# Optimization experiments

Measured on AMD Instinct MI355X. Metric: run time of the kernel, lower is better.

## Reference

```python
import jax, jax.numpy as jnp
import numpy as np

N_NODES = 50000
N_EDGES = 1000000
NODE_F = 64
EDGE_F = 64
OUT_F = 128
K = 2  # matches init k=2


def setup_inputs() -> dict:
    key = jax.random.key(0)
    k1, k2, k3, k4, k5, k6 = jax.random.split(key, 6)
    node_feat = jax.random.normal(k1, (N_NODES, NODE_F), dtype=jnp.float32)
    edge_feat = jax.random.normal(k2, (N_EDGES, EDGE_F), dtype=jnp.float32)
    # nn.Linear(edge_feats*2 + node_feats, out_feats): weight [out, in], bias [out]
    W = jax.random.normal(k3, (OUT_F, 2 * EDGE_F + NODE_F), dtype=jnp.float32) * 0.05
    b = jax.random.normal(k4, (OUT_F,), dtype=jnp.float32) * 0.05
    src = jax.random.randint(k5, (N_EDGES,), 0, N_NODES, dtype=jnp.int64)
    dst = jax.random.randint(k6, (N_EDGES,), 0, N_NODES, dtype=jnp.int64)
    return {"node_feat": node_feat, "edge_feat": edge_feat, "W": W, "b": b,
            "src": src, "dst": dst}


def reference(node_feat, edge_feat, W, b, src, dst):
    N = node_feat.shape[0]
    # norm = in_degrees().clamp(min=1) ** -0.5, shape [N, 1]
    deg = jax.ops.segment_sum(jnp.ones_like(dst, dtype=node_feat.dtype), dst,
                              num_segments=N)
    norm = jnp.maximum(deg, 1.0) ** -0.5
    norm = norm[:, None]
    # DGL semantics: update_all(copy_e, sum) overwrites ndata['h'] with the
    # scatter-sum of edge data over destination nodes; apply_edges then copies
    # the (un-normalized) node 'h' back to edges via edge.src.
    e = edge_feat  # [E, EDGE_F]
    fstack = [node_feat]
    for _ in range(K):
        h = jax.ops.segment_sum(e, dst, num_segments=N)  # [N, EDGE_F]
        fstack.append(h * norm)
        e = h[src]  # apply_edges: e = src node h (un-normalized)
    rst = jnp.concatenate(fstack, axis=-1) @ W.T + b  # [N, OUT_F]
    est = rst[src]  # final apply_edges copies lin output to edges
    return rst, est
```

## Files before the change

### kernel.cpp

```cpp
#include <hip/hip_runtime.h>
#include <hip/hip_bf16.h>

#define NF 64
#define N_OUT 128
#define CAT 192

typedef __attribute__((ext_vector_type(4))) float f32x4;
typedef __attribute__((ext_vector_type(8))) short bf16x8;

__device__ inline short f2bf(float x) {
  unsigned u = __float_as_uint(x);
  unsigned r = (u + 0x7fff + ((u >> 16) & 1)) >> 16;
  return (short)r;
}

__device__ inline f32x4 sx4(f32x4 v, int m) {
  f32x4 r;
  r.x = __shfl_xor(v.x, m, 64);
  r.y = __shfl_xor(v.y, m, 64);
  r.z = __shfl_xor(v.z, m, 64);
  r.w = __shfl_xor(v.w, m, 64);
  return r;
}

__global__ __launch_bounds__(256) void deg_kernel(const int* __restrict__ dst,
                                                  int* __restrict__ deg, int n_edges) {
  int i = blockIdx.x * blockDim.x + threadIdx.x;
  int stride = gridDim.x * blockDim.x;
  for (; i < n_edges; i += stride) {
    int d = __builtin_nontemporal_load(&dst[i]);
    atomicAdd(&deg[d], 1);
  }
}

__global__ __launch_bounds__(256) void scanA_kernel(const int* __restrict__ deg,
                                                    int* __restrict__ offs,
                                                    float* __restrict__ norm,
                                                    int* __restrict__ bsum, int n) {
  int tid = threadIdx.x;
  int i = blockIdx.x * 256 + tid;
  int lane = tid & 63, wid = tid >> 6;
  int v = (i < n) ? deg[i] : 0;
  int s = v;
  #pragma unroll
  for (int o = 1; o < 64; o <<= 1) {
    int t = __shfl_up(s, o, 64);
    if (lane >= o) s += t;
  }
  __shared__ int ws[4], wb[4];
  if (lane == 63) ws[wid] = s;
  __syncthreads();
  if (tid == 0) {
    int run = 0;
    #pragma unroll
    for (int w = 0; w < 4; ++w) { wb[w] = run; run += ws[w]; }
    bsum[blockIdx.x] = run;
  }
  __syncthreads();
  if (i < n) {
    offs[i] = wb[wid] + s - v;
    norm[i] = rsqrtf(fmaxf((float)v, 1.0f));
  }
}

__global__ __launch_bounds__(256) void scanB_kernel(int* __restrict__ bsum, int nb) {
  int tid = threadIdx.x, lane = tid & 63, wid = tid >> 6;
  int v = (tid < nb) ? bsum[tid] : 0;
  int s = v;
  #pragma unroll
  for (int o = 1; o < 64; o <<= 1) {
    int t = __shfl_up(s, o, 64);
    if (lane >= o) s += t;
  }
  __shared__ int ws[4], wb[4];
  if (lane == 63) ws[wid] = s;
  __syncthreads();
  if (tid == 0) {
    int run = 0;
    #pragma unroll
    for (int w = 0; w < 4; ++w) { wb[w] = run; run += ws[w]; }
  }
  __syncthreads();
  if (tid < nb) bsum[tid] = wb[wid] + s - v;
}

__global__ __launch_bounds__(256) void scanC_kernel(int* __restrict__ offs,
                                                    const int* __restrict__ bsum, int n) {
  int i = blockIdx.x * 256 + threadIdx.x;
  if (i < n) offs[i] += bsum[blockIdx.x];
}

__global__ __launch_bounds__(256) void fill_kernel(const int* __restrict__ src,
                                                   const int* __restrict__ dst,
                                                   int* __restrict__ offs,
                                                   int2* __restrict__ csr, int n_edges) {
  int i = blockIdx.x * blockDim.x + threadIdx.x;
  int stride = gridDim.x * blockDim.x;
  for (; i < n_edges; i += stride) {
    int d = __builtin_nontemporal_load(&dst[i]);
    int s = __builtin_nontemporal_load(&src[i]);
    int p = atomicAdd(&offs[d], 1);
    csr[p] = make_int2(i, s);
  }
}

__global__ __launch_bounds__(256) void h1_kernel(const float* __restrict__ edge_feat,
                                                 const int2* __restrict__ csr,
                                                 const int* __restrict__ offs,
                                                 float* __restrict__ h1, int n_nodes) {
  int n = blockIdx.x * 4 + (threadIdx.x >> 6);
  if (n >= n_nodes) return;
  int l = threadIdx.x & 63;
  int l15 = l & 15, l4 = l >> 4;
  int kb = n ? offs[n - 1] : 0;
  int ke = offs[n];
  f32x4 acc0 = {0.f, 0.f, 0.f, 0.f}, acc1 = {0.f, 0.f, 0.f, 0.f};
  int k = kb;
  for (; k + 8 <= ke; k += 8) {
    int e0 = csr[k + l4].x;
    int e1 = csr[k + 4 + l4].x;
    f32x4 v0 = __builtin_nontemporal_load((const f32x4*)&edge_feat[(size_t)e0 * NF + l15 * 4]);
    f32x4 v1 = __builtin_nontemporal_load((const f32x4*)&edge_feat[(size_t)e1 * NF + l15 * 4]);
    acc0 += v0;
    acc1 += v1;
  }
  if (k + 4 <= ke) {
    int e = csr[k + l4].x;
    acc0 += __builtin_nontemporal_load((const f32x4*)&edge_feat[(size_t)e * NF + l15 * 4]);
    k += 4;
  }
  int rem = ke - k;
  if (l4 < rem) {
    int e = csr[k + l4].x;
    acc1 += __builtin_nontemporal_load((const f32x4*)&edge_feat[(size_t)e * NF + l15 * 4]);
  }
  f32x4 t = acc0 + acc1;
  t += sx4(t, 16);
  t += sx4(t, 32);
  if (l4 == 0) *(f32x4*)&h1[(size_t)n * NF + l15 * 4] = t;
}

__global__ __launch_bounds__(256) void h2_kernel(const float* __restrict__ h1,
                                                 const int2* __restrict__ csr,
                                                 const int* __restrict__ offs,
                                                 float* __restrict__ h2, int n_nodes) {
  int n = blockIdx.x * 4 + (threadIdx.x >> 6);
  if (n >= n_nodes) return;
  int l = threadIdx.x & 63;
  int l15 = l & 15, l4 = l >> 4;
  int kb = n ? offs[n - 1] : 0;
  int ke = offs[n];
  f32x4 acc0 = {0.f, 0.f, 0.f, 0.f}, acc1 = {0.f, 0.f, 0.f, 0.f};
  int k = kb;
  for (; k + 8 <= ke; k += 8) {
    int s0 = csr[k + l4].y;
    int s1 = csr[k + 4 + l4].y;
    acc0 += *(const f32x4*)&h1[(size_t)s0 * NF + l15 * 4];
    acc1 += *(const f32x4*)&h1[(size_t)s1 * NF + l15 * 4];
  }
  if (k + 4 <= ke) {
    int s = csr[k + l4].y;
    acc0 += *(const f32x4*)&h1[(size_t)s * NF + l15 * 4];
    k += 4;
  }
  int rem = ke - k;
  if (l4 < rem) {
    int s = csr[k + l4].y;
    acc1 += *(const f32x4*)&h1[(size_t)s * NF + l15 * 4];
  }
  f32x4 t = acc0 + acc1;
  t += sx4(t, 16);
  t += sx4(t, 32);
  if (l4 == 0) *(f32x4*)&h2[(size_t)n * NF + l15 * 4] = t;
}

__global__ __launch_bounds__(256) void gemm_kernel(const float* __restrict__ node_feat,
                                                   const float* __restrict__ h1,
                                                   const float* __restrict__ h2,
                                                   const float* __restrict__ norm,
                                                   const float* __restrict__ W,
                                                   const float* __restrict__ bias,
                                                   float* __restrict__ rst,
                                                   short* __restrict__ rstb, int n_nodes) {
  __shared__ short F[32 * 200];
  __shared__ float R[32][132];
  int tid = threadIdx.x;
  int l = tid & 63, w = tid >> 6;
  int l15 = l & 15, l4 = l >> 4;

  bf16x8 Bf[6][2];
  #pragma unroll
  for (int c = 0; c < 2; ++c) {
    int col = w * 32 + c * 16 + l15;
    const float* wp = &W[(size_t)col * CAT];
    #pragma unroll
    for (int ks = 0; ks < 6; ++ks) {
      int k0 = ks * 32 + l4 * 8;
      bf16x8 b;
      #pragma unroll
      for (int j = 0; j < 8; ++j) b[j] = f2bf(wp[k0 + j]);
      Bf[ks][c] = b;
    }
  }
  float bias0 = bias[w * 32 + l15];
  float bias1 = bias[w * 32 + 16 + l15];

  int tiles = (n_nodes + 31) / 32;
  for (int tile = blockIdx.x; tile < tiles; tile += gridDim.x) {
    int nbase = tile * 32;
    __syncthreads();
    for (int idx = tid; idx < 768; idx += 256) {
      int m = idx / 24, q = idx - m * 24;
      int n = nbase + m;
      bf16x8 pk;
      if (n < n_nodes) {
        const float* sp;
        float scale = 1.f;
        if (q < 8)       sp = &node_feat[(size_t)n * NF + q * 8];
        else if (q < 16) { sp = &h1[(size_t)n * NF + (q - 8) * 8]; scale = norm[n]; }
        else             { sp = &h2[(size_t)n * NF + (q - 16) * 8]; scale = norm[n]; }
        f32x4 v0 = *(const f32x4*)sp;
        f32x4 v1 = *(const f32x4*)(sp + 4);
        pk[0] = f2bf(v0.x * scale); pk[1] = f2bf(v0.y * scale);
        pk[2] = f2bf(v0.z * scale); pk[3] = f2bf(v0.w * scale);
        pk[4] = f2bf(v1.x * scale); pk[5] = f2bf(v1.y * scale);
        pk[6] = f2bf(v1.z * scale); pk[7] = f2bf(v1.w * scale);
      } else {
        pk = bf16x8{0,0,0,0,0,0,0,0};
      }
      *(bf16x8*)&F[m * 200 + q * 8] = pk;
    }
    __syncthreads();
    f32x4 acc00 = {0.f,0.f,0.f,0.f}, acc01 = {0.f,0.f,0.f,0.f};
    f32x4 acc10 = {0.f,0.f,0.f,0.f}, acc11 = {0.f,0.f,0.f,0.f};
    #pragma unroll
    for (int ks = 0; ks < 6; ++ks) {
      bf16x8 a0 = *(const bf16x8*)&F[l15 * 200 + ks * 32 + l4 * 8];
      bf16x8 a1 = *(const bf16x8*)&F[(16 + l15) * 200 + ks * 32 + l4 * 8];
      acc00 = __builtin_amdgcn_mfma_f32_16x16x32_bf16(a0, Bf[ks][0], acc00, 0, 0, 0);
      acc01 = __builtin_amdgcn_mfma_f32_16x16x32_bf16(a0, Bf[ks][1], acc01, 0, 0, 0);
      acc10 = __builtin_amdgcn_mfma_f32_16x16x32_bf16(a1, Bf[ks][0], acc10, 0, 0, 0);
      acc11 = __builtin_amdgcn_mfma_f32_16x16x32_bf16(a1, Bf[ks][1], acc11, 0, 0, 0);
    }
    #pragma unroll
    for (int rt = 0; rt < 2; ++rt) {
      f32x4 ac0 = rt ? acc10 : acc00;
      f32x4 ac1 = rt ? acc11 : acc01;
      #pragma unroll
      for (int r = 0; r < 4; ++r) {
        int row = rt * 16 + l4 * 4 + r;
        R[row][w * 32 + l15] = ac0[r] + bias0;
        R[row][w * 32 + 16 + l15] = ac1[r] + bias1;
      }
    }
    __syncthreads();
    for (int idx = tid; idx < 32 * 32; idx += 256) {
      int m = idx >> 5, c = idx & 31;
      int n = nbase + m;
      if (n < n_nodes) {
        f32x4 v = *(const f32x4*)&R[m][c * 4];
        __builtin_nontemporal_store(v, (f32x4*)&rst[(size_t)n * N_OUT + c * 4]);
      }
    }
    if (rstb) {
      for (int idx = tid; idx < 32 * 16; idx += 256) {
        int m = idx >> 4, q = idx & 15;
        int n = nbase + m;
        if (n < n_nodes) {
          const float* rp = &R[m][q * 8];
          bf16x8 pk;
          #pragma unroll
          for (int j = 0; j < 8; ++j) pk[j] = f2bf(rp[j]);
          *(bf16x8*)&rstb[(size_t)n * N_OUT + q * 8] = pk;
        }
      }
    }
  }
}

__global__ __launch_bounds__(256) void est_bf16_kernel(const short* __restrict__ rstb,
                                                       const int* __restrict__ src,
                                                       float* __restrict__ est, int n_edges) {
  f32x4* e4 = (f32x4*)est;
  int total = n_edges * 32;
  int i = blockIdx.x * blockDim.x + threadIdx.x;
  int stride = gridDim.x * blockDim.x;
  for (; i < total; i += stride) {
    int e = i >> 5, c = i & 31;
    ushort4 b = *(const ushort4*)&rstb[(size_t)src[e] * N_OUT + c * 4];
    f32x4 v;
    v.x = __uint_as_float((unsigned)b.x << 16);
    v.y = __uint_as_float((unsigned)b.y << 16);
    v.z = __uint_as_float((unsigned)b.z << 16);
    v.w = __uint_as_float((unsigned)b.w << 16);
    __builtin_nontemporal_store(v, &e4[i]);
  }
}

__global__ __launch_bounds__(256) void est_f32_kernel(const float* __restrict__ rst,
                                                      const int* __restrict__ src,
                                                      float* __restrict__ est, int n_edges) {
  const f32x4* r4 = (const f32x4*)rst;
  f32x4* e4 = (f32x4*)est;
  int total = n_edges * 32;
  int i = blockIdx.x * blockDim.x + threadIdx.x;
  int stride = gridDim.x * blockDim.x;
  for (; i < total; i += stride) {
    int e = i >> 5, c = i & 31;
    f32x4 v = r4[(size_t)src[e] * 32 + c];
    __builtin_nontemporal_store(v, &e4[i]);
  }
}

extern "C" void kernel_launch(void* const* d_in, const int* in_sizes, int n_in,
                              void* d_out, int out_size, void* d_ws, size_t ws_size,
                              hipStream_t stream) {
  const float* node_feat = (const float*)d_in[0];
  const float* edge_feat = (const float*)d_in[1];
  const float* W = (const float*)d_in[2];
  const float* bias = (const float*)d_in[3];
  const int* src = (const int*)d_in[4];
  const int* dst = (const int*)d_in[5];
  int n_nodes = in_sizes[0] / NF;
  int n_edges = in_sizes[4];

  size_t off = 0;
  auto take = [&](size_t bytes) -> void* {
    void* p = (char*)d_ws + off;
    off += (bytes + 255) & ~(size_t)255;
    return p;
  };
  int* deg = (int*)take((size_t)n_nodes * 4);
  int* offs = (int*)take(((size_t)n_nodes + 1) * 4);
  float* norm = (float*)take((size_t)n_nodes * 4);
  int* bsum = (int*)take(256 * 4);
  int2* csr = (int2*)take((size_t)n_edges * 8);
  float* h1 = (float*)take((size_t)n_nodes * NF * 4);
  float* h2 = (float*)take((size_t)n_nodes * NF * 4);
  size_t rstb_bytes = (size_t)n_nodes * N_OUT * 2;
  short* rstb = nullptr;
  if (off + rstb_bytes <= ws_size) rstb = (short*)take(rstb_bytes);

  float* rst = (float*)d_out;
  float* est = rst + (size_t)n_nodes * N_OUT;

  hipMemsetAsync(deg, 0, (size_t)n_nodes * 4, stream);

  deg_kernel<<<2048, 256, 0, stream>>>(dst, deg, n_edges);
  int nbs = (n_nodes + 255) / 256;
  scanA_kernel<<<nbs, 256, 0, stream>>>(deg, offs, norm, bsum, n_nodes);
  scanB_kernel<<<1, 256, 0, stream>>>(bsum, nbs);
  scanC_kernel<<<nbs, 256, 0, stream>>>(offs, bsum, n_nodes);
  fill_kernel<<<2048, 256, 0, stream>>>(src, dst, offs, csr, n_edges);
  int nb = (n_nodes + 3) / 4;
  h1_kernel<<<nb, 256, 0, stream>>>(edge_feat, csr, offs, h1, n_nodes);
  h2_kernel<<<nb, 256, 0, stream>>>(h1, csr, offs, h2, n_nodes);
  gemm_kernel<<<320, 256, 0, stream>>>(node_feat, h1, h2, norm, W, bias,
                                       rst, rstb, n_nodes);
  if (rstb)
    est_bf16_kernel<<<4096, 256, 0, stream>>>(rstb, src, est, n_edges);
  else
    est_f32_kernel<<<4096, 256, 0, stream>>>(rst, src, est, n_edges);
}
```

Baseline: 389.2 us.

## Fuse scan phases, unroll gathers wider, enlarge GEMM tiles, retune grids

Merges the block-sum scan and offset fixup into one kernel, where each block redundantly rescans the block sums. This removes one launch. Packs CSR entries as 64-bit values written with nontemporal stores. Unrolls the h1/h2 gather loops to 16 edges with four accumulators so more loads are in flight. Doubles the GEMM tile to 64 rows with 512-thread blocks and raises the est grid size, at the cost of more LDS and register pressure per block.

```diff
diff --git a/kernel.cpp b/kernel.cpp
--- a/kernel.cpp
+++ b/kernel.cpp
@@ -63,7 +63,8 @@
   }
 }
 
-__global__ __launch_bounds__(256) void scanB_kernel(int* __restrict__ bsum, int nb) {
+__global__ __launch_bounds__(256) void scanBC_kernel(const int* __restrict__ bsum,
+                                                     int* __restrict__ offs, int n, int nb) {
   int tid = threadIdx.x, lane = tid & 63, wid = tid >> 6;
   int v = (tid < nb) ? bsum[tid] : 0;
   int s = v;
@@ -81,26 +82,25 @@
     for (int w = 0; w < 4; ++w) { wb[w] = run; run += ws[w]; }
   }
   __syncthreads();
-  if (tid < nb) bsum[tid] = wb[wid] + s - v;
-}
-
-__global__ __launch_bounds__(256) void scanC_kernel(int* __restrict__ offs,
-                                                    const int* __restrict__ bsum, int n) {
-  int i = blockIdx.x * 256 + threadIdx.x;
-  if (i < n) offs[i] += bsum[blockIdx.x];
+  __shared__ int sbase;
+  if (tid == blockIdx.x) sbase = wb[wid] + s - v;
+  __syncthreads();
+  int i = blockIdx.x * 256 + tid;
+  if (i < n) offs[i] += sbase;
 }
 
 __global__ __launch_bounds__(256) void fill_kernel(const int* __restrict__ src,
                                                    const int* __restrict__ dst,
                                                    int* __restrict__ offs,
-                                                   int2* __restrict__ csr, int n_edges) {
+                                                   long long* __restrict__ csr, int n_edges) {
   int i = blockIdx.x * blockDim.x + threadIdx.x;
   int stride = gridDim.x * blockDim.x;
   for (; i < n_edges; i += stride) {
     int d = __builtin_nontemporal_load(&dst[i]);
     int s = __builtin_nontemporal_load(&src[i]);
     int p = atomicAdd(&offs[d], 1);
-    csr[p] = make_int2(i, s);
+    long long pk = (long long)(((unsigned long long)(unsigned)s << 32) | (unsigned)i);
+    __builtin_nontemporal_store(pk, &csr[p]);
   }
 }
 
@@ -114,27 +114,37 @@
   int l15 = l & 15, l4 = l >> 4;
   int kb = n ? offs[n - 1] : 0;
   int ke = offs[n];
-  f32x4 acc0 = {0.f, 0.f, 0.f, 0.f}, acc1 = {0.f, 0.f, 0.f, 0.f};
+  f32x4 acc0 = {0.f,0.f,0.f,0.f}, acc1 = {0.f,0.f,0.f,0.f};
+  f32x4 acc2 = {0.f,0.f,0.f,0.f}, acc3 = {0.f,0.f,0.f,0.f};
   int k = kb;
-  for (; k + 8 <= ke; k += 8) {
+  for (; k + 16 <= ke; k += 16) {
     int e0 = csr[k + l4].x;
     int e1 = csr[k + 4 + l4].x;
-    f32x4 v0 = __builtin_nontemporal_load((const f32x4*)&edge_feat[(size_t)e0 * NF + l15 * 4]);
-    f32x4 v1 = __builtin_nontemporal_load((const f32x4*)&edge_feat[(size_t)e1 * NF + l15 * 4]);
-    acc0 += v0;
-    acc1 += v1;
+    int e2 = csr[k + 8 + l4].x;
+    int e3 = csr[k + 12 + l4].x;
+    acc0 += __builtin_nontemporal_load((const f32x4*)&edge_feat[(size_t)e0 * NF + l15 * 4]);
+    acc1 += __builtin_nontemporal_load((const f32x4*)&edge_feat[(size_t)e1 * NF + l15 * 4]);
+    acc2 += __builtin_nontemporal_load((const f32x4*)&edge_feat[(size_t)e2 * NF + l15 * 4]);
+    acc3 += __builtin_nontemporal_load((const f32x4*)&edge_feat[(size_t)e3 * NF + l15 * 4]);
+  }
+  if (k + 8 <= ke) {
+    int e0 = csr[k + l4].x;
+    int e1 = csr[k + 4 + l4].x;
+    acc0 += __builtin_nontemporal_load((const f32x4*)&edge_feat[(size_t)e0 * NF + l15 * 4]);
+    acc1 += __builtin_nontemporal_load((const f32x4*)&edge_feat[(size_t)e1 * NF + l15 * 4]);
+    k += 8;
   }
   if (k + 4 <= ke) {
     int e = csr[k + l4].x;
-    acc0 += __builtin_nontemporal_load((const f32x4*)&edge_feat[(size_t)e * NF + l15 * 4]);
+    acc2 += __builtin_nontemporal_load((const f32x4*)&edge_feat[(size_t)e * NF + l15 * 4]);
     k += 4;
   }
   int rem = ke - k;
   if (l4 < rem) {
     int e = csr[k + l4].x;
-    acc1 += __builtin_nontemporal_load((const f32x4*)&edge_feat[(size_t)e * NF + l15 * 4]);
-  }
-  f32x4 t = acc0 + acc1;
+    acc3 += __builtin_nontemporal_load((const f32x4*)&edge_feat[(size_t)e * NF + l15 * 4]);
+  }
+  f32x4 t = (acc0 + acc1) + (acc2 + acc3);
   t += sx4(t, 16);
   t += sx4(t, 32);
   if (l4 == 0) *(f32x4*)&h1[(size_t)n * NF + l15 * 4] = t;
@@ -150,31 +160,43 @@
   int l15 = l & 15, l4 = l >> 4;
   int kb = n ? offs[n - 1] : 0;
   int ke = offs[n];
-  f32x4 acc0 = {0.f, 0.f, 0.f, 0.f}, acc1 = {0.f, 0.f, 0.f, 0.f};
+  f32x4 acc0 = {0.f,0.f,0.f,0.f}, acc1 = {0.f,0.f,0.f,0.f};
+  f32x4 acc2 = {0.f,0.f,0.f,0.f}, acc3 = {0.f,0.f,0.f,0.f};
   int k = kb;
-  for (; k + 8 <= ke; k += 8) {
+  for (; k + 16 <= ke; k += 16) {
+    int s0 = csr[k + l4].y;
+    int s1 = csr[k + 4 + l4].y;
+    int s2 = csr[k + 8 + l4].y;
+    int s3 = csr[k + 12 + l4].y;
+    acc0 += *(const f32x4*)&h1[(size_t)s0 * NF + l15 * 4];
+    acc1 += *(const f32x4*)&h1[(size_t)s1 * NF + l15 * 4];
+    acc2 += *(const f32x4*)&h1[(size_t)s2 * NF + l15 * 4];
+    acc3 += *(const f32x4*)&h1[(size_t)s3 * NF + l15 * 4];
+  }
+  if (k + 8 <= ke) {
     int s0 = csr[k + l4].y;
     int s1 = csr[k + 4 + l4].y;
     acc0 += *(const f32x4*)&h1[(size_t)s0 * NF + l15 * 4];
     acc1 += *(const f32x4*)&h1[(size_t)s1 * NF + l15 * 4];
+    k += 8;
   }
   if (k + 4 <= ke) {
     int s = csr[k + l4].y;
-    acc0 += *(const f32x4*)&h1[(size_t)s * NF + l15 * 4];
+    acc2 += *(const f32x4*)&h1[(size_t)s * NF + l15 * 4];
     k += 4;
   }
   int rem = ke - k;
   if (l4 < rem) {
     int s = csr[k + l4].y;
-    acc1 += *(const f32x4*)&h1[(size_t)s * NF + l15 * 4];
-  }
-  f32x4 t = acc0 + acc1;
+    acc3 += *(const f32x4*)&h1[(size_t)s * NF + l15 * 4];
+  }
+  f32x4 t = (acc0 + acc1) + (acc2 + acc3);
   t += sx4(t, 16);
   t += sx4(t, 32);
   if (l4 == 0) *(f32x4*)&h2[(size_t)n * NF + l15 * 4] = t;
 }
 
-__global__ __launch_bounds__(256) void gemm_kernel(const float* __restrict__ node_feat,
+__global__ __launch_bounds__(512) void gemm_kernel(const float* __restrict__ node_feat,
                                                    const float* __restrict__ h1,
                                                    const float* __restrict__ h2,
                                                    const float* __restrict__ norm,
@@ -182,16 +204,17 @@
                                                    const float* __restrict__ bias,
                                                    float* __restrict__ rst,
                                                    short* __restrict__ rstb, int n_nodes) {
-  __shared__ short F[32 * 200];
-  __shared__ float R[32][132];
+  __shared__ short F[64 * 200];
+  __shared__ float R[64][132];
   int tid = threadIdx.x;
   int l = tid & 63, w = tid >> 6;
+  int w2 = w & 3, wh = w >> 2;
   int l15 = l & 15, l4 = l >> 4;
 
   bf16x8 Bf[6][2];
   #pragma unroll
   for (int c = 0; c < 2; ++c) {
-    int col = w * 32 + c * 16 + l15;
+    int col = w2 * 32 + c * 16 + l15;
     const float* wp = &W[(size_t)col * CAT];
     #pragma unroll
     for (int ks = 0; ks < 6; ++ks) {
@@ -202,14 +225,14 @@
       Bf[ks][c] = b;
     }
   }
-  float bias0 = bias[w * 32 + l15];
-  float bias1 = bias[w * 32 + 16 + l15];
-
-  int tiles = (n_nodes + 31) / 32;
+  float bias0 = bias[w2 * 32 + l15];
+  float bias1 = bias[w2 * 32 + 16 + l15];
+
+  int tiles = (n_nodes + 63) / 64;
   for (int tile = blockIdx.x; tile < tiles; tile += gridDim.x) {
-    int nbase = tile * 32;
+    int nbase = tile * 64;
     __syncthreads();
-    for (int idx = tid; idx < 768; idx += 256) {
+    for (int idx = tid; idx < 1536; idx += 512) {
       int m = idx / 24, q = idx - m * 24;
       int n = nbase + m;
       bf16x8 pk;
@@ -235,8 +258,8 @@
     f32x4 acc10 = {0.f,0.f,0.f,0.f}, acc11 = {0.f,0.f,0.f,0.f};
     #pragma unroll
     for (int ks = 0; ks < 6; ++ks) {
-      bf16x8 a0 = *(const bf16x8*)&F[l15 * 200 + ks * 32 + l4 * 8];
-      bf16x8 a1 = *(const bf16x8*)&F[(16 + l15) * 200 + ks * 32 + l4 * 8];
+      bf16x8 a0 = *(const bf16x8*)&F[(wh * 32 + l15) * 200 + ks * 32 + l4 * 8];
+      bf16x8 a1 = *(const bf16x8*)&F[(wh * 32 + 16 + l15) * 200 + ks * 32 + l4 * 8];
       acc00 = __builtin_amdgcn_mfma_f32_16x16x32_bf16(a0, Bf[ks][0], acc00, 0, 0, 0);
       acc01 = __builtin_amdgcn_mfma_f32_16x16x32_bf16(a0, Bf[ks][1], acc01, 0, 0, 0);
       acc10 = __builtin_amdgcn_mfma_f32_16x16x32_bf16(a1, Bf[ks][0], acc10, 0, 0, 0);
@@ -248,13 +271,13 @@
       f32x4 ac1 = rt ? acc11 : acc01;
       #pragma unroll
       for (int r = 0; r < 4; ++r) {
-        int row = rt * 16 + l4 * 4 + r;
-        R[row][w * 32 + l15] = ac0[r] + bias0;
-        R[row][w * 32 + 16 + l15] = ac1[r] + bias1;
+        int row = wh * 32 + rt * 16 + l4 * 4 + r;
+        R[row][w2 * 32 + l15] = ac0[r] + bias0;
+        R[row][w2 * 32 + 16 + l15] = ac1[r] + bias1;
       }
     }
     __syncthreads();
-    for (int idx = tid; idx < 32 * 32; idx += 256) {
+    for (int idx = tid; idx < 64 * 32; idx += 512) {
       int m = idx >> 5, c = idx & 31;
       int n = nbase + m;
       if (n < n_nodes) {
@@ -263,7 +286,7 @@
       }
     }
     if (rstb) {
-      for (int idx = tid; idx < 32 * 16; idx += 256) {
+      for (int idx = tid; idx < 64 * 16; idx += 512) {
         int m = idx >> 4, q = idx & 15;
         int n = nbase + m;
         if (n < n_nodes) {
@@ -334,7 +357,7 @@
   int* offs = (int*)take(((size_t)n_nodes + 1) * 4);
   float* norm = (float*)take((size_t)n_nodes * 4);
   int* bsum = (int*)take(256 * 4);
-  int2* csr = (int2*)take((size_t)n_edges * 8);
+  long long* csr = (long long*)take((size_t)n_edges * 8);
   float* h1 = (float*)take((size_t)n_nodes * NF * 4);
   float* h2 = (float*)take((size_t)n_nodes * NF * 4);
   size_t rstb_bytes = (size_t)n_nodes * N_OUT * 2;
@@ -344,21 +367,20 @@
   float* rst = (float*)d_out;
   float* est = rst + (size_t)n_nodes * N_OUT;
 
-  hipMemsetAsync(deg, 0, (size_t)n_nodes * 4, stream);
+  (void)hipMemsetAsync(deg, 0, (size_t)n_nodes * 4, stream);
 
   deg_kernel<<<2048, 256, 0, stream>>>(dst, deg, n_edges);
   int nbs = (n_nodes + 255) / 256;
   scanA_kernel<<<nbs, 256, 0, stream>>>(deg, offs, norm, bsum, n_nodes);
-  scanB_kernel<<<1, 256, 0, stream>>>(bsum, nbs);
-  scanC_kernel<<<nbs, 256, 0, stream>>>(offs, bsum, n_nodes);
+  scanBC_kernel<<<nbs, 256, 0, stream>>>(bsum, offs, n_nodes, nbs);
   fill_kernel<<<2048, 256, 0, stream>>>(src, dst, offs, csr, n_edges);
   int nb = (n_nodes + 3) / 4;
-  h1_kernel<<<nb, 256, 0, stream>>>(edge_feat, csr, offs, h1, n_nodes);
-  h2_kernel<<<nb, 256, 0, stream>>>(h1, csr, offs, h2, n_nodes);
-  gemm_kernel<<<320, 256, 0, stream>>>(node_feat, h1, h2, norm, W, bias,
+  h1_kernel<<<nb, 256, 0, stream>>>(edge_feat, (const int2*)csr, offs, h1, n_nodes);
+  h2_kernel<<<nb, 256, 0, stream>>>(h1, (const int2*)csr, offs, h2, n_nodes);
+  gemm_kernel<<<512, 512, 0, stream>>>(node_feat, h1, h2, norm, W, bias,
                                        rst, rstb, n_nodes);
   if (rstb)
-    est_bf16_kernel<<<4096, 256, 0, stream>>>(rstb, src, est, n_edges);
+    est_bf16_kernel<<<8192, 256, 0, stream>>>(rstb, src, est, n_edges);
   else
-    est_f32_kernel<<<4096, 256, 0, stream>>>(rst, src, est, n_edges);
-}
+    est_f32_kernel<<<8192, 256, 0, stream>>>(rst, src, est, n_edges);
+}
```

New measurement: 382.8 us. No clear change (-1.7%).
